# Kernel optimization log

Measured on AMD Instinct MI355X. Metric: run time of the kernel, lower is better.

Reference implementation:

```python
import jax, jax.numpy as jnp
import numpy as np

HEADS = 8
DIM_HEAD = 64


def setup_inputs() -> dict:
    key = jax.random.key(0)
    ks = jax.random.split(key, 6)
    b, dim, h, w = 8, 512, 64, 64
    inner = HEADS * DIM_HEAD  # 512
    return {
        "f_m": jax.random.normal(ks[0], (b, dim, h, w), dtype=jnp.float32),
        "f_n": jax.random.normal(ks[1], (b, dim, h, w), dtype=jnp.float32),
        "Wq": jax.random.normal(ks[2], (inner, dim), dtype=jnp.float32) * 0.02,
        "Wkv": jax.random.normal(ks[3], (2 * inner, dim), dtype=jnp.float32) * 0.02,
        "Wout": jax.random.normal(ks[4], (dim, inner), dtype=jnp.float32) * 0.02,
        "bout": jax.random.normal(ks[5], (dim,), dtype=jnp.float32) * 0.02,
    }


def reference(f_m, f_n, Wq, Wkv, Wout, bout):
    b, c, h, w = f_m.shape
    n = h * w
    scale = DIM_HEAD ** -0.5
    # 1x1 convs == channel GEMMs
    q = jnp.einsum('oc,bchw->bohw', Wq, f_m).reshape(b, HEADS, DIM_HEAD, n)
    kv = jnp.einsum('oc,bchw->bohw', Wkv, f_n)
    k, v = jnp.split(kv, 2, axis=1)
    k = k.reshape(b, HEADS, DIM_HEAD, n)
    v = v.reshape(b, HEADS, DIM_HEAD, n)
    # NOTE: contraction is over spatial n -> channel attention [b,h,d,d]
    dots = jnp.einsum('bhin,bhjn->bhij', q, k) * scale
    attn = jax.nn.softmax(dots, axis=-1)
    out = jnp.einsum('bhij,bhjn->bhin', attn, v).reshape(b, HEADS * DIM_HEAD, h, w)
    return jnp.einsum('oc,bchw->bohw', Wout, out) + bout[None, :, None, None]
```

## Files before the change

kernel.cpp:

```cpp
#include <hip/hip_runtime.h>
#include <hip/hip_bf16.h>
#include <stdint.h>

typedef __bf16 bf16_t;
typedef __bf16 bf16x8 __attribute__((ext_vector_type(8)));
typedef float f32x4 __attribute__((ext_vector_type(4)));

#define MFMA_16x16x32(A, B, C) __builtin_amdgcn_mfma_f32_16x16x32_bf16((A), (B), (C), 0, 0, 0)

__device__ inline void gload_lds16(const bf16_t* g, bf16_t* lds) {
  auto* gp = (const __attribute__((address_space(1))) uint32_t*)(uintptr_t)g;
  auto* lp = (__attribute__((address_space(3))) uint32_t*)(uintptr_t)lds;
  __builtin_amdgcn_global_load_lds(gp, lp, 16, 0, 0);
}

__global__ __launch_bounds__(512, 2)
void k_front(const float* __restrict__ f_m, const float* __restrict__ f_n,
             const float* __restrict__ Wq, const float* __restrict__ Wkv,
             const float* __restrict__ Wout,
             bf16_t* __restrict__ Hp, bf16_t* __restrict__ fnT,
             bf16_t* __restrict__ wq_b, bf16_t* __restrict__ wk_b,
             bf16_t* __restrict__ wout_b, bf16_t* __restrict__ wvT) {
  __shared__ __align__(16) char ldsbuf[65536];
  const int bid = blockIdx.x;
  const int tid = threadIdx.x;

  if (bid < 256) {
    const int xcd = bid & 7, idx = bid >> 3;
    const int mt = idx & 1, nt = (idx >> 1) & 1, ks = idx >> 2;
    const int b = xcd;
    const float* Ab = f_n + (size_t)b * 512 * 4096;
    const float* Bb = f_m + (size_t)b * 512 * 4096;
    const int bm = mt * 256, bn = nt * 256;
    const int kbeg = ks * 512;

    const int wave = tid >> 6, lane = tid & 63;
    const int l15 = lane & 15, l4 = lane >> 4;
    const int wm = (wave >> 2) * 128, wn = (wave & 3) * 64;
    const int rsw = (l15 >> 1) & 3;

    bf16_t* As0 = (bf16_t*)ldsbuf;
    bf16_t* Bs0 = As0 + 16384;

    f32x4 acc[8][4] = {};

    const int rho = tid >> 1, h = tid & 1;
    const int sw = (rho >> 1) & 3;
    const int wo0 = rho * 32 + (((2 * h) ^ sw) * 8);
    const int wo1 = rho * 32 + (((2 * h + 1) ^ sw) * 8);
    const float* ga = Ab + (size_t)(bm + rho) * 4096 + kbeg + h * 16;
    const float* gb = Bb + (size_t)(bn + rho) * 4096 + kbeg + h * 16;

    float4 ra[4], rb[4];
#pragma unroll
    for (int q = 0; q < 4; ++q) {
      ra[q] = *(const float4*)(ga + q * 4);
      rb[q] = *(const float4*)(gb + q * 4);
    }

    int cur = 0;
    for (int i = 0; i < 16; ++i) {
      bf16_t* As = As0 + cur * 8192;
      bf16_t* Bs = Bs0 + cur * 8192;
      bf16_t ta[16], tb[16];
#pragma unroll
      for (int q = 0; q < 4; ++q) {
        ta[q * 4 + 0] = (bf16_t)ra[q].x; ta[q * 4 + 1] = (bf16_t)ra[q].y;
        ta[q * 4 + 2] = (bf16_t)ra[q].z; ta[q * 4 + 3] = (bf16_t)ra[q].w;
        tb[q * 4 + 0] = (bf16_t)rb[q].x; tb[q * 4 + 1] = (bf16_t)rb[q].y;
        tb[q * 4 + 2] = (bf16_t)rb[q].z; tb[q * 4 + 3] = (bf16_t)rb[q].w;
      }
      *(uint4*)(&As[wo0]) = *(uint4*)(ta);
      *(uint4*)(&As[wo1]) = *(uint4*)(ta + 8);
      *(uint4*)(&Bs[wo0]) = *(uint4*)(tb);
      *(uint4*)(&Bs[wo1]) = *(uint4*)(tb + 8);
      if (i + 1 < 16) {
        const float* na = ga + (i + 1) * 32;
        const float* nb = gb + (i + 1) * 32;
#pragma unroll
        for (int q = 0; q < 4; ++q) {
          ra[q] = *(const float4*)(na + q * 4);
          rb[q] = *(const float4*)(nb + q * 4);
        }
      }
      __syncthreads();
      bf16x8 bfr[4];
#pragma unroll
      for (int n = 0; n < 4; ++n)
        bfr[n] = *(const bf16x8*)(&Bs[(wn + n * 16 + l15) * 32 + ((l4 ^ rsw) * 8)]);
#pragma unroll
      for (int m = 0; m < 8; ++m) {
        bf16x8 af = *(const bf16x8*)(&As[(wm + m * 16 + l15) * 32 + ((l4 ^ rsw) * 8)]);
#pragma unroll
        for (int n = 0; n < 4; ++n)
          acc[m][n] = MFMA_16x16x32(af, bfr[n], acc[m][n]);
      }
      cur ^= 1;
    }

    bf16_t* Cb = Hp + (size_t)(b * 8 + ks) * 262144;
#pragma unroll
    for (int m = 0; m < 8; ++m) {
      const int row0 = bm + wm + m * 16 + l4 * 4;
#pragma unroll
      for (int n = 0; n < 4; ++n) {
        const int col = bn + wn + n * 16 + l15;
#pragma unroll
        for (int j = 0; j < 4; ++j)
          Cb[(size_t)(row0 + j) * 512 + col] = (bf16_t)acc[m][n][j];
      }
    }
  } else if (bid < 2304) {
    const int half = tid >> 8;
    const int t = tid & 255;
    const int tileIdx = (bid - 256) * 2 + half;
    const int ntile = tileIdx & 63, ctile = (tileIdx >> 6) & 7, b = tileIdx >> 9;
    const int C = 512, N = 4096;
    const float* src = f_n + (size_t)b * C * N;
    const int n0 = ntile * 64, c0 = ctile * 64;
    float* tile = (float*)ldsbuf + half * (64 * 65);

    const int cr = t >> 2;
    const int nc = (t & 3) * 16;
    {
      const float* srow = src + (size_t)(c0 + cr) * N + n0 + nc;
#pragma unroll
      for (int q = 0; q < 4; ++q) {
        float4 v = *(const float4*)(srow + q * 4);
        tile[cr * 65 + nc + q * 4 + 0] = v.x; tile[cr * 65 + nc + q * 4 + 1] = v.y;
        tile[cr * 65 + nc + q * 4 + 2] = v.z; tile[cr * 65 + nc + q * 4 + 3] = v.w;
      }
    }
    __syncthreads();
    {
      const int nr = t >> 2;
      const int cc = (t & 3) * 16;
      bf16_t on[16];
#pragma unroll
      for (int q = 0; q < 16; ++q) on[q] = (bf16_t)tile[(cc + q) * 65 + nr];
      bf16_t* dst = fnT + (size_t)b * (size_t)N * C + (size_t)(n0 + nr) * C + c0 + cc;
      *(uint4*)(dst) = *(uint4*)(on);
      *(uint4*)(dst + 8) = *(uint4*)(on + 8);
    }
  } else if (bid < 2688) {
    int i = (bid - 2304) * 512 + tid;
    int region = i >> 16;
    int e = (i & 65535) * 4;
    const float* src = region == 0 ? Wq : (region == 1 ? Wkv : Wout);
    bf16_t* dst = region == 0 ? wq_b : (region == 1 ? wk_b : wout_b);
    float4 v = *(const float4*)(src + e);
    bf16_t o[4] = {(bf16_t)v.x, (bf16_t)v.y, (bf16_t)v.z, (bf16_t)v.w};
    *(uint2*)(dst + e) = *(uint2*)o;
  } else {
    const int half = tid >> 8;
    const int t = tid & 255;
    const int tileIdx = (bid - 2688) * 2 + half;
    const int x = tileIdx & 15, yy = (tileIdx >> 4) & 1, z = tileIdx >> 5;
    const int C = 64, N = 512;
    const float* src = Wkv + (size_t)512 * 512 + (size_t)z * C * N;
    bf16_t* dst = wvT + (size_t)z * C * N;
    const int n0 = x * 32, c0 = yy * 32;
    float* tile = (float*)ldsbuf + half * (32 * 33);
    const int tx = t & 31, ty = (t >> 5) & 7;
#pragma unroll
    for (int i = 0; i < 32; i += 8)
      tile[(ty + i) * 33 + tx] = src[(size_t)(c0 + ty + i) * N + (n0 + tx)];
    __syncthreads();
#pragma unroll
    for (int i = 0; i < 32; i += 8)
      dst[(size_t)(n0 + ty + i) * C + (c0 + tx)] = (bf16_t)tile[tx * 33 + ty + i];
  }
}

__global__ __launch_bounds__(256)
void k_reduce8(const bf16_t* __restrict__ p, bf16_t* __restrict__ out) {
  int i = blockIdx.x * blockDim.x + threadIdx.x;
  int b = i >> 15;
  int e8 = (i & 32767) * 8;
  const bf16_t* pb = p + (size_t)b * 8 * 262144 + e8;
  float s[8] = {};
#pragma unroll
  for (int ks = 0; ks < 8; ++ks) {
    bf16x8 v = *(const bf16x8*)(pb + (size_t)ks * 262144);
#pragma unroll
    for (int j = 0; j < 8; ++j) s[j] += (float)v[j];
  }
  bf16x8 o;
#pragma unroll
  for (int j = 0; j < 8; ++j) o[j] = (bf16_t)s[j];
  *(bf16x8*)(out + (size_t)b * 262144 + e8) = o;
}

__global__ __launch_bounds__(256)
void k_gemm_bt(const bf16_t* __restrict__ A, const bf16_t* __restrict__ B,
               bf16_t* __restrict__ Cv, int M, int N, int K,
               long long sA, long long sB, long long sC) {
  const int zb = blockIdx.z;
  A += (size_t)zb * sA;
  B += (size_t)zb * sB;

  const int tid = threadIdx.x;
  const int wave = tid >> 6, lane = tid & 63;
  const int l15 = lane & 15, l4 = lane >> 4;
  const int bm = blockIdx.y * 128, bn = blockIdx.x * 128;
  const int wm = (wave >> 1) * 64, wn = (wave & 1) * 64;

  __shared__ bf16_t As[2][128 * 32];
  __shared__ bf16_t Bs[2][128 * 32];

  f32x4 acc[4][4] = {};

  const int lrow = lane >> 2;
  const int lchunk = (lane & 3) * 8;
  const int ra = wave * 16 + lrow;

  auto stage = [&](int buf, int k0) {
    gload_lds16(&A[(size_t)(bm + ra) * K + k0 + lchunk],      &As[buf][(wave * 16) * 32]);
    gload_lds16(&A[(size_t)(bm + 64 + ra) * K + k0 + lchunk], &As[buf][(64 + wave * 16) * 32]);
    gload_lds16(&B[(size_t)(bn + ra) * K + k0 + lchunk],      &Bs[buf][(wave * 16) * 32]);
    gload_lds16(&B[(size_t)(bn + 64 + ra) * K + k0 + lchunk], &Bs[buf][(64 + wave * 16) * 32]);
  };

  const int nsteps = K / 32;
  stage(0, 0);
  __syncthreads();

  for (int i = 0; i < nsteps; ++i) {
    const int cur = i & 1;
    if (i + 1 < nsteps) stage(cur ^ 1, (i + 1) * 32);
    bf16x8 af[4], bfr[4];
#pragma unroll
    for (int m = 0; m < 4; ++m)
      af[m] = *(const bf16x8*)(&As[cur][(wm + m * 16 + l15) * 32 + l4 * 8]);
#pragma unroll
    for (int n = 0; n < 4; ++n)
      bfr[n] = *(const bf16x8*)(&Bs[cur][(wn + n * 16 + l15) * 32 + l4 * 8]);
#pragma unroll
    for (int m = 0; m < 4; ++m)
#pragma unroll
      for (int n = 0; n < 4; ++n)
        acc[m][n] = MFMA_16x16x32(af[m], bfr[n], acc[m][n]);
    __syncthreads();
  }

#pragma unroll
  for (int m = 0; m < 4; ++m) {
    const int row0 = bm + wm + m * 16 + l4 * 4;
#pragma unroll
    for (int n = 0; n < 4; ++n) {
      const int col = bn + wn + n * 16 + l15;
#pragma unroll
      for (int j = 0; j < 4; ++j)
        (Cv + (size_t)zb * sC)[(size_t)(row0 + j) * N + col] = (bf16_t)acc[m][n][j];
    }
  }
}

__global__ __launch_bounds__(256)
void k_dots_wveff(const bf16_t* __restrict__ T1, const bf16_t* __restrict__ wk,
                  const bf16_t* __restrict__ wvT, bf16_t* __restrict__ wveffT) {
  const int bh = blockIdx.x;
  const int b = bh >> 3, hh = bh & 7;
  const bf16_t* qh = T1 + (size_t)b * 262144 + (size_t)hh * 64 * 512;
  const bf16_t* kh = wk + (size_t)hh * 64 * 512;
  const int tid = threadIdx.x;
  const int wave = tid >> 6, lane = tid & 63;
  const int l15 = lane & 15, l4 = lane >> 4;

  __shared__ float S[64][65];
  __shared__ bf16_t P[64][72];

  {
    const int wm = (wave >> 1) * 32, wn = (wave & 1) * 32;
    f32x4 acc[2][2] = {};
#pragma unroll 2
    for (int k0 = 0; k0 < 512; k0 += 32) {
      bf16x8 af[2], bfr[2];
#pragma unroll
      for (int m = 0; m < 2; ++m)
        af[m] = *(const bf16x8*)(&qh[(size_t)(wm + m * 16 + l15) * 512 + k0 + l4 * 8]);
#pragma unroll
      for (int n = 0; n < 2; ++n)
        bfr[n] = *(const bf16x8*)(&kh[(size_t)(wn + n * 16 + l15) * 512 + k0 + l4 * 8]);
#pragma unroll
      for (int m = 0; m < 2; ++m)
#pragma unroll
        for (int n = 0; n < 2; ++n)
          acc[m][n] = MFMA_16x16x32(af[m], bfr[n], acc[m][n]);
    }
    const float scale = 0.125f;
#pragma unroll
    for (int m = 0; m < 2; ++m)
#pragma unroll
      for (int n = 0; n < 2; ++n)
#pragma unroll
        for (int j = 0; j < 4; ++j)
          S[wm + m * 16 + l4 * 4 + j][wn + n * 16 + l15] = acc[m][n][j] * scale;
  }
  __syncthreads();

  {
    const int r = tid >> 2, seg = (tid & 3) * 16;
    float vals[16];
    float mx = -1e30f;
#pragma unroll
    for (int c = 0; c < 16; ++c) { vals[c] = S[r][seg + c]; mx = fmaxf(mx, vals[c]); }
    mx = fmaxf(mx, __shfl_xor(mx, 1));
    mx = fmaxf(mx, __shfl_xor(mx, 2));
    float sum = 0.f;
#pragma unroll
    for (int c = 0; c < 16; ++c) { vals[c] = __expf(vals[c] - mx); sum += vals[c]; }
    sum += __shfl_xor(sum, 1);
    sum += __shfl_xor(sum, 2);
    const float inv = 1.0f / sum;
    bf16_t pr[16];
#pragma unroll
    for (int c = 0; c < 16; ++c) pr[c] = (bf16_t)(vals[c] * inv);
    *(uint4*)(&P[r][seg]) = *(uint4*)(pr);
    *(uint4*)(&P[r][seg + 8]) = *(uint4*)(pr + 8);
  }
  __syncthreads();

  {
    const bf16_t* av = wvT + (size_t)hh * 512 * 64;
    bf16_t* ob = wveffT + (size_t)b * 262144 + (size_t)hh * 64;
    const int wm = (wave >> 1) * 64, wn = (wave & 1) * 32;
    for (int cm0 = 0; cm0 < 512; cm0 += 128) {
      f32x4 acc[4][2] = {};
#pragma unroll
      for (int ks = 0; ks < 2; ++ks) {
        const int k0 = ks * 32;
        bf16x8 af[4], bfr[2];
#pragma unroll
        for (int m = 0; m < 4; ++m)
          af[m] = *(const bf16x8*)(&av[(size_t)(cm0 + wm + m * 16 + l15) * 64 + k0 + l4 * 8]);
#pragma unroll
        for (int n = 0; n < 2; ++n)
          bfr[n] = *(const bf16x8*)(&P[wn + n * 16 + l15][k0 + l4 * 8]);
#pragma unroll
        for (int m = 0; m < 4; ++m)
#pragma unroll
          for (int n = 0; n < 2; ++n)
            acc[m][n] = MFMA_16x16x32(af[m], bfr[n], acc[m][n]);
      }
#pragma unroll
      for (int m = 0; m < 4; ++m)
#pragma unroll
        for (int n = 0; n < 2; ++n)
#pragma unroll
          for (int j = 0; j < 4; ++j)
            ob[(size_t)(cm0 + wm + m * 16 + l4 * 4 + j) * 512 + wn + n * 16 + l15] =
                (bf16_t)acc[m][n][j];
    }
  }
}

__global__ __launch_bounds__(512, 2)
void k_y256(const bf16_t* __restrict__ A, const bf16_t* __restrict__ B,
            float* __restrict__ C, const float* __restrict__ bias) {
  const int raw = blockIdx.x;
  const int b = raw & 7, c = raw >> 3;
  const int bm = (c & 1) * 256, bn = (c >> 1) * 256;
  A += (size_t)b * 262144;
  B += (size_t)b * 4096 * 512;
  C += (size_t)b * 512 * 4096;

  const int tid = threadIdx.x;
  const int wave = tid >> 6, lane = tid & 63;
  const int l15 = lane & 15, l4 = lane >> 4;
  const int wm = (wave >> 2) * 128, wn = (wave & 3) * 64;
  const int rsw = (l15 >> 1) & 3;

  __shared__ bf16_t As[2][256 * 32];
  __shared__ bf16_t Bs[2][256 * 32];

  f32x4 acc[8][4] = {};

  const int lrow = lane >> 2;
  const int lch = (lane & 3) ^ ((lane >> 3) & 3);
  const bf16_t* srcA = A + (size_t)(bm + wave * 32 + lrow) * 512 + lch * 8;
  const bf16_t* srcB = B + (size_t)(bn + wave * 32 + lrow) * 512 + lch * 8;
  bf16_t* dstA = &As[0][wave * 32 * 32];
  bf16_t* dstB = &Bs[0][wave * 32 * 32];
  const int bufoff = 256 * 32;

  auto stage = [&](int buf, int k0) {
    gload_lds16(srcA + k0,            dstA + buf * bufoff);
    gload_lds16(srcA + 16 * 512 + k0, dstA + buf * bufoff + 512);
    gload_lds16(srcB + k0,            dstB + buf * bufoff);
    gload_lds16(srcB + 16 * 512 + k0, dstB + buf * bufoff + 512);
  };

  stage(0, 0);
  __syncthreads();

  int cur = 0;
  for (int i = 0; i < 16; ++i) {
    if (i + 1 < 16) stage(cur ^ 1, (i + 1) * 32);
    bf16x8 bfr[4];
#pragma unroll
    for (int n = 0; n < 4; ++n)
      bfr[n] = *(const bf16x8*)(&Bs[cur][(wn + n * 16 + l15) * 32 + ((l4 ^ rsw) * 8)]);
#pragma unroll
    for (int m = 0; m < 8; ++m) {
      bf16x8 af = *(const bf16x8*)(&As[cur][(wm + m * 16 + l15) * 32 + ((l4 ^ rsw) * 8)]);
#pragma unroll
      for (int n = 0; n < 4; ++n)
        acc[m][n] = MFMA_16x16x32(af, bfr[n], acc[m][n]);
    }
    __syncthreads();
    cur ^= 1;
  }

#pragma unroll
  for (int m = 0; m < 8; ++m) {
    const int row0 = bm + wm + m * 16 + l4 * 4;
#pragma unroll
    for (int n = 0; n < 4; ++n) {
      const int col = bn + wn + n * 16 + l15;
#pragma unroll
      for (int j = 0; j < 4; ++j)
        C[(size_t)(row0 + j) * 4096 + col] = acc[m][n][j] + bias[row0 + j];
    }
  }
}

extern "C" void kernel_launch(void* const* d_in, const int* in_sizes, int n_in,
                              void* d_out, int out_size, void* d_ws, size_t ws_size,
                              hipStream_t stream) {
  const float* f_m  = (const float*)d_in[0];
  const float* f_n  = (const float*)d_in[1];
  const float* Wq   = (const float*)d_in[2];
  const float* Wkv  = (const float*)d_in[3];
  const float* Wout = (const float*)d_in[4];
  const float* bout = (const float*)d_in[5];
  float* y = (float*)d_out;

  const size_t ACT = (size_t)8 * 4096 * 512;
  const size_t SQ  = (size_t)512 * 512;
  char* p = (char*)d_ws;
  bf16_t* wq_b    = (bf16_t*)p; p += SQ * 2;
  bf16_t* wk_b    = (bf16_t*)p; p += SQ * 2;
  bf16_t* wout_b  = (bf16_t*)p; p += SQ * 2;
  bf16_t* wvT     = (bf16_t*)p; p += SQ * 2;
  bf16_t* Hb      = (bf16_t*)p; p += (size_t)8 * SQ * 2;
  bf16_t* T1      = (bf16_t*)p; p += (size_t)8 * SQ * 2;
  bf16_t* wveffT  = (bf16_t*)p; p += (size_t)8 * SQ * 2;
  bf16_t* W2      = (bf16_t*)p; p += (size_t)8 * SQ * 2;
  bf16_t* Hp8     = (bf16_t*)p; p += (size_t)64 * SQ * 2;
  bf16_t* fnT     = (bf16_t*)p; p += ACT * 2;

  k_front<<<dim3(2816), 512, 0, stream>>>(f_m, f_n, Wq, Wkv, Wout,
                                          Hp8, fnT, wq_b, wk_b, wout_b, wvT);
  k_reduce8<<<dim3(1024), 256, 0, stream>>>(Hp8, Hb);

  k_gemm_bt<<<dim3(4, 4, 8), 256, 0, stream>>>(wq_b, Hb, T1, 512, 512, 512,
                                               0, (long long)SQ, (long long)SQ);
  k_dots_wveff<<<dim3(64), 256, 0, stream>>>(T1, wk_b, wvT, wveffT);
  k_gemm_bt<<<dim3(4, 4, 8), 256, 0, stream>>>(wout_b, wveffT, W2, 512, 512, 512,
                                               0, (long long)SQ, (long long)SQ);
  k_y256<<<dim3(256), 512, 0, stream>>>(W2, fnT, y, bout);
}
```

Baseline: 127.6 us.

## Fuse f_n transpose and bf16 cast into final output GEMM

Removes the separate k_front stage that transposed f_n to a bf16 [n,c] buffer. The final GEMM now reads fp32 f_n directly, transposes and converts it through an LDS staging tile, and uses a smaller 256x128 output tile with 512 blocks. This avoids writing and re-reading the 32 MB bf16 intermediate. In exchange it adds register-staged B loads, two extra barriers per k-step, and halves the per-block tile, which reduces reuse of A.

Result: faster. 115.5 us (-9.4%).

```diff
diff --git a/kernel.cpp b/kernel.cpp
--- a/kernel.cpp
+++ b/kernel.cpp
@@ -18,7 +18,7 @@
 void k_front(const float* __restrict__ f_m, const float* __restrict__ f_n,
              const float* __restrict__ Wq, const float* __restrict__ Wkv,
              const float* __restrict__ Wout,
-             bf16_t* __restrict__ Hp, bf16_t* __restrict__ fnT,
+             bf16_t* __restrict__ Hp,
              bf16_t* __restrict__ wq_b, bf16_t* __restrict__ wk_b,
              bf16_t* __restrict__ wout_b, bf16_t* __restrict__ wvT) {
   __shared__ __align__(16) char ldsbuf[65536];
@@ -110,40 +110,8 @@
           Cb[(size_t)(row0 + j) * 512 + col] = (bf16_t)acc[m][n][j];
       }
     }
-  } else if (bid < 2304) {
-    const int half = tid >> 8;
-    const int t = tid & 255;
-    const int tileIdx = (bid - 256) * 2 + half;
-    const int ntile = tileIdx & 63, ctile = (tileIdx >> 6) & 7, b = tileIdx >> 9;
-    const int C = 512, N = 4096;
-    const float* src = f_n + (size_t)b * C * N;
-    const int n0 = ntile * 64, c0 = ctile * 64;
-    float* tile = (float*)ldsbuf + half * (64 * 65);
-
-    const int cr = t >> 2;
-    const int nc = (t & 3) * 16;
-    {
-      const float* srow = src + (size_t)(c0 + cr) * N + n0 + nc;
-#pragma unroll
-      for (int q = 0; q < 4; ++q) {
-        float4 v = *(const float4*)(srow + q * 4);
-        tile[cr * 65 + nc + q * 4 + 0] = v.x; tile[cr * 65 + nc + q * 4 + 1] = v.y;
-        tile[cr * 65 + nc + q * 4 + 2] = v.z; tile[cr * 65 + nc + q * 4 + 3] = v.w;
-      }
-    }
-    __syncthreads();
-    {
-      const int nr = t >> 2;
-      const int cc = (t & 3) * 16;
-      bf16_t on[16];
-#pragma unroll
-      for (int q = 0; q < 16; ++q) on[q] = (bf16_t)tile[(cc + q) * 65 + nr];
-      bf16_t* dst = fnT + (size_t)b * (size_t)N * C + (size_t)(n0 + nr) * C + c0 + cc;
-      *(uint4*)(dst) = *(uint4*)(on);
-      *(uint4*)(dst + 8) = *(uint4*)(on + 8);
-    }
-  } else if (bid < 2688) {
-    int i = (bid - 2304) * 512 + tid;
+  } else if (bid < 640) {
+    int i = (bid - 256) * 512 + tid;
     int region = i >> 16;
     int e = (i & 65535) * 4;
     const float* src = region == 0 ? Wq : (region == 1 ? Wkv : Wout);
@@ -154,7 +122,7 @@
   } else {
     const int half = tid >> 8;
     const int t = tid & 255;
-    const int tileIdx = (bid - 2688) * 2 + half;
+    const int tileIdx = (bid - 640) * 2 + half;
     const int x = tileIdx & 15, yy = (tileIdx >> 4) & 1, z = tileIdx >> 5;
     const int C = 64, N = 512;
     const float* src = Wkv + (size_t)512 * 512 + (size_t)z * C * N;
@@ -356,64 +324,81 @@
 }
 
 __global__ __launch_bounds__(512, 2)
-void k_y256(const bf16_t* __restrict__ A, const bf16_t* __restrict__ B,
+void k_yf32(const bf16_t* __restrict__ A, const float* __restrict__ Bf,
             float* __restrict__ C, const float* __restrict__ bias) {
   const int raw = blockIdx.x;
   const int b = raw & 7, c = raw >> 3;
-  const int bm = (c & 1) * 256, bn = (c >> 1) * 256;
-  A += (size_t)b * 262144;
-  B += (size_t)b * 4096 * 512;
-  C += (size_t)b * 512 * 4096;
+  const int bm = (c & 1) * 256, bn = (c >> 1) * 128;
+  A  += (size_t)b * 262144;
+  Bf += (size_t)b * 512 * 4096;
+  C  += (size_t)b * 512 * 4096;
 
   const int tid = threadIdx.x;
   const int wave = tid >> 6, lane = tid & 63;
   const int l15 = lane & 15, l4 = lane >> 4;
-  const int wm = (wave >> 2) * 128, wn = (wave & 3) * 64;
+  const int wm = (wave >> 1) * 64, wn = (wave & 1) * 64;
   const int rsw = (l15 >> 1) & 3;
 
   __shared__ bf16_t As[2][256 * 32];
-  __shared__ bf16_t Bs[2][256 * 32];
-
-  f32x4 acc[8][4] = {};
+  __shared__ bf16_t Bs[2][128 * 32];
+  __shared__ float  Ft[32 * 128];
+
+  f32x4 acc[4][4] = {};
 
   const int lrow = lane >> 2;
   const int lch = (lane & 3) ^ ((lane >> 3) & 3);
   const bf16_t* srcA = A + (size_t)(bm + wave * 32 + lrow) * 512 + lch * 8;
-  const bf16_t* srcB = B + (size_t)(bn + wave * 32 + lrow) * 512 + lch * 8;
   bf16_t* dstA = &As[0][wave * 32 * 32];
-  bf16_t* dstB = &Bs[0][wave * 32 * 32];
-  const int bufoff = 256 * 32;
-
-  auto stage = [&](int buf, int k0) {
-    gload_lds16(srcA + k0,            dstA + buf * bufoff);
-    gload_lds16(srcA + 16 * 512 + k0, dstA + buf * bufoff + 512);
-    gload_lds16(srcB + k0,            dstB + buf * bufoff);
-    gload_lds16(srcB + 16 * 512 + k0, dstB + buf * bufoff + 512);
-  };
-
-  stage(0, 0);
+  const int bufA = 256 * 32;
+
+  const int fr = tid >> 4, fc = (tid & 15) * 8;
+  const float* srcB = Bf + (size_t)fr * 4096 + bn + fc;
+
+  const int tn = tid >> 2, tc = (tid & 3) * 8;
+  const int wchunk = ((tid & 3) ^ ((tn >> 1) & 3)) * 8;
+
+  float4 rb0 = *(const float4*)(srcB);
+  float4 rb1 = *(const float4*)(srcB + 4);
+  gload_lds16(srcA, dstA);
+  gload_lds16(srcA + 16 * 512, dstA + 512);
   __syncthreads();
 
   int cur = 0;
   for (int i = 0; i < 16; ++i) {
-    if (i + 1 < 16) stage(cur ^ 1, (i + 1) * 32);
-    bf16x8 bfr[4];
+    *(float4*)(&Ft[fr * 128 + fc]) = rb0;
+    *(float4*)(&Ft[fr * 128 + fc + 4]) = rb1;
+    __syncthreads();
+    {
+      bf16_t tb[8];
+#pragma unroll
+      for (int q = 0; q < 8; ++q) tb[q] = (bf16_t)Ft[(tc + q) * 128 + tn];
+      *(uint4*)(&Bs[cur][tn * 32 + wchunk]) = *(uint4*)tb;
+    }
+    __syncthreads();
+    if (i + 1 < 16) {
+      const float* nb = srcB + (size_t)(i + 1) * 32 * 4096;
+      rb0 = *(const float4*)(nb);
+      rb1 = *(const float4*)(nb + 4);
+      gload_lds16(srcA + (i + 1) * 32,            dstA + (cur ^ 1) * bufA);
+      gload_lds16(srcA + 16 * 512 + (i + 1) * 32, dstA + (cur ^ 1) * bufA + 512);
+    }
+    bf16x8 af[4], bfr[4];
 #pragma unroll
     for (int n = 0; n < 4; ++n)
       bfr[n] = *(const bf16x8*)(&Bs[cur][(wn + n * 16 + l15) * 32 + ((l4 ^ rsw) * 8)]);
 #pragma unroll
-    for (int m = 0; m < 8; ++m) {
-      bf16x8 af = *(const bf16x8*)(&As[cur][(wm + m * 16 + l15) * 32 + ((l4 ^ rsw) * 8)]);
+    for (int m = 0; m < 4; ++m)
+      af[m] = *(const bf16x8*)(&As[cur][(wm + m * 16 + l15) * 32 + ((l4 ^ rsw) * 8)]);
+#pragma unroll
+    for (int m = 0; m < 4; ++m)
 #pragma unroll
       for (int n = 0; n < 4; ++n)
-        acc[m][n] = MFMA_16x16x32(af, bfr[n], acc[m][n]);
-    }
-    __syncthreads();
+        acc[m][n] = MFMA_16x16x32(af[m], bfr[n], acc[m][n]);
     cur ^= 1;
   }
 
 #pragma unroll
-  for (int m = 0; m < 8; ++m) {
+  for (int m = 0; m < 4; ++m) {
     const int row0 = bm + wm + m * 16 + l4 * 4;
 #pragma unroll
     for (int n = 0; n < 4; ++n) {
@@ -436,7 +421,6 @@
   const float* bout = (const float*)d_in[5];
   float* y = (float*)d_out;
 
-  const size_t ACT = (size_t)8 * 4096 * 512;
   const size_t SQ  = (size_t)512 * 512;
   char* p = (char*)d_ws;
   bf16_t* wq_b    = (bf16_t*)p; p += SQ * 2;
@@ -448,10 +432,9 @@
   bf16_t* wveffT  = (bf16_t*)p; p += (size_t)8 * SQ * 2;
   bf16_t* W2      = (bf16_t*)p; p += (size_t)8 * SQ * 2;
   bf16_t* Hp8     = (bf16_t*)p; p += (size_t)64 * SQ * 2;
-  bf16_t* fnT     = (bf16_t*)p; p += ACT * 2;
-
-  k_front<<<dim3(2816), 512, 0, stream>>>(f_m, f_n, Wq, Wkv, Wout,
-                                          Hp8, fnT, wq_b, wk_b, wout_b, wvT);
+
+  k_front<<<dim3(768), 512, 0, stream>>>(f_m, f_n, Wq, Wkv, Wout,
+                                         Hp8, wq_b, wk_b, wout_b, wvT);
   k_reduce8<<<dim3(1024), 256, 0, stream>>>(Hp8, Hb);
 
   k_gemm_bt<<<dim3(4, 4, 8), 256, 0, stream>>>(wq_b, Hb, T1, 512, 512, 512,
@@ -459,5 +442,5 @@
   k_dots_wveff<<<dim3(64), 256, 0, stream>>>(T1, wk_b, wvT, wveffT);
   k_gemm_bt<<<dim3(4, 4, 8), 256, 0, stream>>>(wout_b, wveffT, W2, 512, 512, 512,
                                                0, (long long)SQ, (long long)SQ);
-  k_y256<<<dim3(256), 512, 0, stream>>>(W2, fnT, y, bout);
-}
+  k_yf32<<<dim3(512), 512, 0, stream>>>(W2, f_n, y, bout);
+}
```
